# Kernel optimization log

Hardware: AMD Instinct MI355X
Metric: run time of the kernel (lower is better)

## Reference

```python
import jax, jax.numpy as jnp
import numpy as np

N_NODES = 100000
N_EDGES = 800000


def gcn_layer(x, W, b, src, dst, n):
    # PyG GCNConv (normalize=True): x @ W, add self-loops, sym-normalized mean aggregation, + bias
    h = x @ W  # [N, out]
    deg = jax.ops.segment_sum(jnp.ones_like(src, dtype=h.dtype), dst, num_segments=n)
    dinv = jnp.where(deg > 0, jax.lax.rsqrt(jnp.maximum(deg, 1.0)), 0.0)
    norm = dinv[src] * dinv[dst]  # [E+N]
    msg = h[src] * norm[:, None]  # gather + scale
    out = jax.ops.segment_sum(msg, dst, num_segments=n)  # scatter-add
    return out + b


def setup_inputs() -> dict:
    key = jax.random.key(0)
    k1, k2, k3, k4 = jax.random.split(key, 4)
    x = jax.random.normal(k1, (N_NODES, 128), dtype=jnp.float32)
    edge_index = jax.random.randint(k2, (2, N_EDGES), 0, N_NODES, dtype=jnp.int64)
    W1 = jax.random.normal(k3, (128, 64), dtype=jnp.float32) * (1.0 / np.sqrt(128))
    b1 = jnp.zeros((64,), dtype=jnp.float32)
    W2 = jax.random.normal(k4, (64, 40), dtype=jnp.float32) * (1.0 / np.sqrt(64))
    b2 = jnp.zeros((40,), dtype=jnp.float32)
    return {"x": x, "edge_index": edge_index, "W1": W1, "b1": b1, "W2": W2, "b2": b2}


def reference(x, edge_index, W1, b1, W2, b2):
    n = x.shape[0]
    loop = jnp.arange(n, dtype=edge_index.dtype)
    src = jnp.concatenate([edge_index[0], loop])  # add self-loops
    dst = jnp.concatenate([edge_index[1], loop])
    h = jax.nn.relu(gcn_layer(x, W1, b1, src, dst, n))
    # dropout is identity in eval mode (self.training=False)
    out = gcn_layer(h, W2, b2, src, dst, n)
    return jax.nn.log_softmax(out, axis=1)
```

## Files before the change

kernel.cpp:

```cpp
#include <hip/hip_runtime.h>
#include <hip/hip_fp16.h>
#include <math.h>


typedef _Float16 f16x8 __attribute__((ext_vector_type(8)));
typedef float    f32x4 __attribute__((ext_vector_type(4)));

__global__ void zero_kernel(int* __restrict__ p, int n) {
    int i = blockIdx.x * blockDim.x + threadIdx.x;
    if (i < n) p[i] = 0;
}

static __device__ __forceinline__ void gemm1_tile(const float* __restrict__ X,
                                                  const float* __restrict__ W,
                                                  _Float16* __restrict__ H, int n,
                                                  int tile, _Float16* Ws ) {
    int t = threadIdx.x;
    int rowbase = tile * 64;

    for (int i = t; i < 2048; i += 256) {
        int k = i >> 4;
        int nn0 = (i & 15) * 4;
        float4 v = *reinterpret_cast<const float4*>(W + (size_t)k * 64 + nn0);
        const float* vp = reinterpret_cast<const float*>(&v);
#pragma unroll
        for (int j = 0; j < 4; ++j) {
            int nn = nn0 + j;
            Ws[nn * 128 + (k ^ ((nn & 7) << 3))] = (_Float16)vp[j];
        }
    }

    int w = t >> 6;
    int l = t & 63;
    int lr = l & 15;
    int lk = l >> 4;
    int arow = rowbase + 16 * w + lr;
    int ar = arow < n ? arow : n - 1;

    f16x8 a[4];
#pragma unroll
    for (int kc = 0; kc < 4; ++kc) {
        const float* xp = X + (size_t)ar * 128 + kc * 32 + lk * 8;
        float4 v0 = *reinterpret_cast<const float4*>(xp);
        float4 v1 = *reinterpret_cast<const float4*>(xp + 4);
        f16x8 hv = { (_Float16)v0.x, (_Float16)v0.y, (_Float16)v0.z, (_Float16)v0.w,
                     (_Float16)v1.x, (_Float16)v1.y, (_Float16)v1.z, (_Float16)v1.w };
        a[kc] = hv;
    }
    __syncthreads();

    f32x4 acc[4] = {};
#pragma unroll
    for (int nt = 0; nt < 4; ++nt) {
        int nrow = 16 * nt + lr;
#pragma unroll
        for (int kc = 0; kc < 4; ++kc) {
            int k8 = kc * 32 + lk * 8;
            f16x8 b = *reinterpret_cast<f16x8*>(&Ws[nrow * 128 + (k8 ^ ((nrow & 7) << 3))]);
            acc[nt] = __builtin_amdgcn_mfma_f32_16x16x32_f16(a[kc], b, acc[nt], 0, 0, 0);
        }
    }
#pragma unroll
    for (int nt = 0; nt < 4; ++nt) {
#pragma unroll
        for (int r = 0; r < 4; ++r) {
            int grow = rowbase + 16 * w + lk * 4 + r;
            if (grow < n) H[(size_t)grow * 64 + nt * 16 + lr] = (_Float16)acc[nt][r];
        }
    }
}

__global__ __launch_bounds__(256) void degrank_gemm1_kernel(
        const int* __restrict__ dst, int* __restrict__ degi, int* __restrict__ rank, int E,
        const float* __restrict__ X, const float* __restrict__ W,
        _Float16* __restrict__ H, int n, int nDeg) {
    __shared__ _Float16 Ws[64 * 128];
    int b = blockIdx.x;
    if (b < nDeg) {
        int base = b * 1024 + threadIdx.x;
        int d[4]; bool v[4];
#pragma unroll
        for (int u = 0; u < 4; ++u) {
            int e = base + u * 256;
            v[u] = e < E;
            d[u] = v[u] ? dst[e] : 0;
        }
        int r[4];
#pragma unroll
        for (int u = 0; u < 4; ++u)
            if (v[u]) r[u] = atomicAdd(&degi[d[u]], 1);
#pragma unroll
        for (int u = 0; u < 4; ++u)
            if (v[u]) rank[base + u * 256] = r[u];
    } else {
        gemm1_tile(X, W, H, n, b - nDeg, Ws);
    }
}

__global__ __launch_bounds__(256) void fill_gemm1_kernel(
        const int* __restrict__ src, const int* __restrict__ dst,
        const int* __restrict__ rank, const float* __restrict__ dinv,
        const int* __restrict__ rowstart, int2* __restrict__ csr, int E,
        const float* __restrict__ X, const float* __restrict__ W,
        _Float16* __restrict__ H, int n, int nFill, int tileOff) {
    __shared__ _Float16 Ws[64 * 128];
    int b = blockIdx.x;
    if (b < nFill) {
        int e = b * 256 + threadIdx.x;
        if (e >= E) return;
        int s = src[e], t = dst[e];
        float nrm = dinv[s] * dinv[t];
        unsigned short us = __half_as_ushort(__float2half_rn(nrm));
        int packed = (int)(((unsigned)us << 16) | us);
        int pos = rowstart[t] + rank[e];
        csr[pos] = make_int2(s, packed);
    } else {
        gemm1_tile(X, W, H, n, b - nFill + tileOff, Ws);
    }
}

__global__ __launch_bounds__(256) void blocksum_kernel(const int* __restrict__ degi,
                                                       int* __restrict__ partial, int n) {
    __shared__ int sm[256];
    int t = threadIdx.x;
    int base = blockIdx.x * 1024 + t * 4;
    int s = 0;
#pragma unroll
    for (int j = 0; j < 4; ++j) { int i = base + j; if (i < n) s += degi[i]; }
    sm[t] = s;
    __syncthreads();
    for (int off = 128; off > 0; off >>= 1) {
        if (t < off) sm[t] += sm[t + off];
        __syncthreads();
    }
    if (t == 0) partial[blockIdx.x] = sm[0];
}

__global__ __launch_bounds__(256) void offsets_kernel(int* __restrict__ degi,
                                                      const int* __restrict__ partial,
                                                      int* __restrict__ rowstart,
                                                      int n, int nb) {
    __shared__ int sm[256];
    __shared__ int pbase_s;
    int t = threadIdx.x;
    int pv = (t < nb) ? partial[t] : 0;
    sm[t] = pv;
    __syncthreads();
    for (int off = 1; off < 256; off <<= 1) {
        int x = (t >= off) ? sm[t - off] : 0;
        __syncthreads();
        sm[t] += x;
        __syncthreads();
    }
    if (t == 0) pbase_s = (blockIdx.x > 0) ? sm[blockIdx.x - 1] : 0;
    __syncthreads();
    int pbase = pbase_s;
    __syncthreads();

    int base = blockIdx.x * 1024 + t * 4;
    int v[4]; int s = 0;
#pragma unroll
    for (int j = 0; j < 4; ++j) { v[j] = (base + j < n) ? degi[base + j] : 0; s += v[j]; }
    sm[t] = s;
    __syncthreads();
    for (int off = 1; off < 256; off <<= 1) {
        int x = (t >= off) ? sm[t - off] : 0;
        __syncthreads();
        sm[t] += x;
        __syncthreads();
    }
    int run = pbase + (sm[t] - s);
#pragma unroll
    for (int j = 0; j < 4; ++j) {
        if (base + j < n) {
            rowstart[base + j] = run; run += v[j];
            ((float*)degi)[base + j] = rsqrtf((float)v[j] + 1.0f);
        }
    }
}

static __device__ __forceinline__ __half2 relu_h2(__half2 v) {
    unsigned u = *reinterpret_cast<unsigned*>(&v);
    unsigned neg = (u >> 15) & 0x00010001u;
    u &= ~(neg * 0xFFFFu);
    return *reinterpret_cast<__half2*>(&u);
}

template <bool RELU, bool BIAS>
__global__ __launch_bounds__(256) void gather64h_kernel(const __half* __restrict__ Hh,
                                                        const int2* __restrict__ csr,
                                                        const int* __restrict__ rowstart,
                                                        const float* __restrict__ dinv,
                                                        const float* __restrict__ b,
                                                        __half* __restrict__ Oh, int n, int E) {
    int gt = blockIdx.x * blockDim.x + threadIdx.x;
    int node = gt >> 3;
    if (node >= n) return;
    int fl = gt & 7;
    const float4* H4 = reinterpret_cast<const float4*>(Hh);
    int rs = rowstart[node];
    int re = (node + 1 < n) ? rowstart[node + 1] : E;
    __half2 acc[4];
#pragma unroll
    for (int q = 0; q < 4; ++q) acc[q] = __float2half2_rn(0.0f);

    int e = rs;
    while (__any(e < re)) {
        int srcrow[4]; __half2 nh[4]; float4 raw[4];
#pragma unroll
        for (int u = 0; u < 4; ++u) {
            int ee = e + u;
            bool valid = ee < re;
            int2 c = csr[valid ? ee : rs];
            srcrow[u] = valid ? c.x : 0;
            int ni = valid ? c.y : 0;
            nh[u] = *reinterpret_cast<__half2*>(&ni);
        }
#pragma unroll
        for (int u = 0; u < 4; ++u)
            raw[u] = H4[srcrow[u] * 8 + fl];
#pragma unroll
        for (int u = 0; u < 4; ++u) {
            const __half2* hp = reinterpret_cast<const __half2*>(&raw[u]);
#pragma unroll
            for (int q = 0; q < 4; ++q)
                acc[q] = __hfma2(hp[q], nh[u], acc[q]);
        }
        e += 4;
    }
    {
        float di = dinv[node];
        __half2 d2 = __float2half2_rn(di * di);
        float4 raw = H4[node * 8 + fl];
        const __half2* hp = reinterpret_cast<const __half2*>(&raw);
#pragma unroll
        for (int q = 0; q < 4; ++q) acc[q] = __hfma2(hp[q], d2, acc[q]);
    }
    if (BIAS) {
        float4 b0 = reinterpret_cast<const float4*>(b)[fl * 2];
        float4 b1 = reinterpret_cast<const float4*>(b)[fl * 2 + 1];
        acc[0] = __hadd2(acc[0], __float22half2_rn(make_float2(b0.x, b0.y)));
        acc[1] = __hadd2(acc[1], __float22half2_rn(make_float2(b0.z, b0.w)));
        acc[2] = __hadd2(acc[2], __float22half2_rn(make_float2(b1.x, b1.y)));
        acc[3] = __hadd2(acc[3], __float22half2_rn(make_float2(b1.z, b1.w)));
    }
    if (RELU) {
#pragma unroll
        for (int q = 0; q < 4; ++q) acc[q] = relu_h2(acc[q]);
    }
    float4 o;
    __half2* op = reinterpret_cast<__half2*>(&o);
#pragma unroll
    for (int q = 0; q < 4; ++q) op[q] = acc[q];
    *reinterpret_cast<float4*>(Oh + (size_t)node * 64 + fl * 8) = o;
}

__global__ __launch_bounds__(256) void gather_gemm2_softmax(
        const __half* __restrict__ Hh, const int2* __restrict__ csr,
        const int* __restrict__ rowstart, const float* __restrict__ dinv,
        const float* __restrict__ W, const float* __restrict__ b,
        float* __restrict__ out, int n, int E) {
    constexpr int BM = 64, K = 64, C = 40, XP = 68, HP = 41;
    __shared__ float Xs[BM * XP];
    __shared__ float Ws[K * C];
    __shared__ float bs[C];
    __shared__ float rowm[BM], rowls[BM];
    int t = threadIdx.x;
    int rowbase = blockIdx.x * BM;

    for (int i = t; i < K * C / 4; i += 256)
        ((float4*)Ws)[i] = ((const float4*)W)[i];
    if (t < C) bs[t] = b[t];

    int team = t >> 3, fl = t & 7;
    const float4* H4 = reinterpret_cast<const float4*>(Hh);
#pragma unroll
    for (int pass = 0; pass < 2; ++pass) {
        int lrow = team + pass * 32;
        int node = rowbase + lrow;
        __half2 acc[4];
#pragma unroll
        for (int q = 0; q < 4; ++q) acc[q] = __float2half2_rn(0.0f);
        if (node < n) {
            int rs = rowstart[node];
            int re = (node + 1 < n) ? rowstart[node + 1] : E;
            int e = rs;
            while (__any(e < re)) {
                int srcrow[4]; __half2 nh[4]; float4 raw[4];
#pragma unroll
                for (int u = 0; u < 4; ++u) {
                    int ee = e + u;
                    bool valid = ee < re;
                    int2 c = csr[valid ? ee : rs];
                    srcrow[u] = valid ? c.x : 0;
                    int ni = valid ? c.y : 0;
                    nh[u] = *reinterpret_cast<__half2*>(&ni);
                }
#pragma unroll
                for (int u = 0; u < 4; ++u)
                    raw[u] = H4[srcrow[u] * 8 + fl];
#pragma unroll
                for (int u = 0; u < 4; ++u) {
                    const __half2* hp = reinterpret_cast<const __half2*>(&raw[u]);
#pragma unroll
                    for (int q = 0; q < 4; ++q)
                        acc[q] = __hfma2(hp[q], nh[u], acc[q]);
                }
                e += 4;
            }
            float di = dinv[node];
            __half2 d2 = __float2half2_rn(di * di);
            float4 raw = H4[node * 8 + fl];
            const __half2* hp = reinterpret_cast<const __half2*>(&raw);
#pragma unroll
            for (int q = 0; q < 4; ++q) acc[q] = __hfma2(hp[q], d2, acc[q]);
        }
        float* dp = &Xs[lrow * XP + fl * 8];
        float2 f0 = __half22float2(acc[0]), f1 = __half22float2(acc[1]);
        float2 f2 = __half22float2(acc[2]), f3 = __half22float2(acc[3]);
        *reinterpret_cast<float4*>(dp)     = make_float4(f0.x, f0.y, f1.x, f1.y);
        *reinterpret_cast<float4*>(dp + 4) = make_float4(f2.x, f2.y, f3.x, f3.y);
    }
    __syncthreads();

    int tx = t % (C / 4);
    int ty = t / (C / 4);
    bool active = ty < BM / 4;
    float acc[4][4] = {};
    if (active) {
#pragma unroll
        for (int k0 = 0; k0 < K; k0 += 4) {
            float4 xq[4], wq[4];
#pragma unroll
            for (int i = 0; i < 4; ++i)
                xq[i] = *reinterpret_cast<const float4*>(&Xs[(ty * 4 + i) * XP + k0]);
#pragma unroll
            for (int j = 0; j < 4; ++j)
                wq[j] = *reinterpret_cast<const float4*>(&Ws[(k0 + j) * C + tx * 4]);
#pragma unroll
            for (int i = 0; i < 4; ++i) {
                const float* xa = reinterpret_cast<const float*>(&xq[i]);
#pragma unroll
                for (int j = 0; j < 4; ++j) {
                    const float* wb = reinterpret_cast<const float*>(&wq[j]);
                    acc[i][0] += xa[j] * wb[0];
                    acc[i][1] += xa[j] * wb[1];
                    acc[i][2] += xa[j] * wb[2];
                    acc[i][3] += xa[j] * wb[3];
                }
            }
        }
    }
    __syncthreads();
    float* Hs = Xs;
    if (active) {
#pragma unroll
        for (int i = 0; i < 4; ++i) {
            int r = ty * 4 + i;
#pragma unroll
            for (int j = 0; j < 4; ++j)
                Hs[r * HP + tx * 4 + j] = acc[i][j] + bs[tx * 4 + j];
        }
    }
    __syncthreads();
    if (t < BM) {
        float m = -INFINITY;
        for (int j = 0; j < C; ++j) m = fmaxf(m, Hs[t * HP + j]);
        float s = 0.f;
        for (int j = 0; j < C; ++j) s += __expf(Hs[t * HP + j] - m);
        rowm[t] = m; rowls[t] = __logf(s);
    }
    __syncthreads();
    for (int idx = t; idx < BM * C; idx += 256) {
        int r = idx / C, c = idx - r * C;
        int gr = rowbase + r;
        if (gr < n) out[(size_t)gr * C + c] = Hs[r * HP + c] - rowm[r] - rowls[r];
    }
}

extern "C" void kernel_launch(void* const* d_in, const int* in_sizes, int n_in,
                              void* d_out, int out_size, void* d_ws, size_t ws_size,
                              hipStream_t stream) {
    const float* x  = (const float*)d_in[0];
    const int*   ei = (const int*)d_in[1];
    const float* W1 = (const float*)d_in[2];
    const float* b1 = (const float*)d_in[3];
    const float* W2 = (const float*)d_in[4];
    const float* b2 = (const float*)d_in[5];
    float* out = (float*)d_out;

    const int n = in_sizes[0] / 128;
    const int E = in_sizes[1] / 2;
    const int* src = ei;
    const int* dst = ei + E;

    auto al = [](size_t x) { return (x + 255) & ~(size_t)255; };
    float* ws = (float*)d_ws;
    size_t o_deg  = 0;
    size_t o_cnt  = al(n);
    size_t o_part = o_cnt + al(n);
    size_t o_rank = o_part + 1024;
    size_t o_csr  = o_rank + al(E);
    size_t o_h1   = o_csr + al((size_t)2 * E);
    size_t o_out1 = o_h1 + al((size_t)n * 32);

    int*    degi     = (int*)(ws + o_deg);
    float*  dinv     = (float*)(ws + o_deg);
    int*    rowstart = (int*)(ws + o_cnt);
    int*    partial  = (int*)(ws + o_part);
    int*    rank     = (int*)(ws + o_rank);
    int2*   csr      = (int2*)(ws + o_csr);
    __half* h1       = (__half*)(ws + o_h1);
    __half* out1     = (__half*)(ws + o_out1);

    const int NB = (n + 1023) / 1024;
    const int nDeg   = (E + 1023) / 1024;
    const int nFill  = (E + 255) / 256;
    const int ntiles = (n + 63) / 64;
    const int tilesA = ntiles / 2;
    const int tilesB = ntiles - tilesA;

    zero_kernel<<<(n + 255) / 256, 256, 0, stream>>>(degi, n);
    degrank_gemm1_kernel<<<nDeg + tilesA, 256, 0, stream>>>(
        dst, degi, rank, E, x, W1, (_Float16*)h1, n, nDeg);
    blocksum_kernel<<<NB, 256, 0, stream>>>(degi, partial, n);
    offsets_kernel<<<NB, 256, 0, stream>>>(degi, partial, rowstart, n, NB);
    fill_gemm1_kernel<<<nFill + tilesB, 256, 0, stream>>>(
        src, dst, rank, dinv, rowstart, csr, E, x, W1, (_Float16*)h1, n, nFill, tilesA);
    gather64h_kernel<true, true><<<((size_t)n * 8 + 255) / 256, 256, 0, stream>>>(
        h1, csr, rowstart, dinv, b1, out1, n, E);
    gather_gemm2_softmax<<<(n + 63) / 64, 256, 0, stream>>>(
        out1, csr, rowstart, dinv, W2, b2, out, n, E);
}
```

Baseline: 136.7 us.

## Privatize degree histogram per XCD with workgroup-scope atomics

Replaces the single global degree histogram with eight per-XCD copies, chosen via the hardware XCC id register. Atomics use workgroup scope so they can stay in the local XCD L2 instead of going device-coherent. A later pass combines the per-XCD counts into totals and per-XCD base offsets, and the CSR fill adds the XCD base to each edge's local rank, which is stored with the XCD id in its top bits. This adds 8x histogram zeroing and a reduction pass, plus extra memory traffic, in exchange for cheaper atomics.

```diff
diff --git a/kernel.cpp b/kernel.cpp
--- a/kernel.cpp
+++ b/kernel.cpp
@@ -5,6 +5,10 @@
 
 typedef _Float16 f16x8 __attribute__((ext_vector_type(8)));
 typedef float    f32x4 __attribute__((ext_vector_type(4)));
+
+static __device__ __forceinline__ int xcd_id() {
+    return __builtin_amdgcn_s_getreg((3 << 11) | 20) & 7;
+}
 
 __global__ void zero_kernel(int* __restrict__ p, int n) {
     int i = blockIdx.x * blockDim.x + threadIdx.x;
@@ -71,12 +75,14 @@
 }
 
 __global__ __launch_bounds__(256) void degrank_gemm1_kernel(
-        const int* __restrict__ dst, int* __restrict__ degi, int* __restrict__ rank, int E,
-        const float* __restrict__ X, const float* __restrict__ W,
-        _Float16* __restrict__ H, int n, int nDeg) {
+        const int* __restrict__ dst, int* __restrict__ degi_x, int* __restrict__ rank,
+        int E, int n, const float* __restrict__ X, const float* __restrict__ W,
+        _Float16* __restrict__ H, int nDeg) {
     __shared__ _Float16 Ws[64 * 128];
     int b = blockIdx.x;
     if (b < nDeg) {
+        int x = xcd_id();
+        int* hist = degi_x + (size_t)x * n;
         int base = b * 1024 + threadIdx.x;
         int d[4]; bool v[4];
 #pragma unroll
@@ -88,21 +94,98 @@
         int r[4];
 #pragma unroll
         for (int u = 0; u < 4; ++u)
-            if (v[u]) r[u] = atomicAdd(&degi[d[u]], 1);
+            if (v[u]) r[u] = __hip_atomic_fetch_add(&hist[d[u]], 1, __ATOMIC_RELAXED,
+                                                    __HIP_MEMORY_SCOPE_WORKGROUP);
 #pragma unroll
         for (int u = 0; u < 4; ++u)
-            if (v[u]) rank[base + u * 256] = r[u];
+            if (v[u]) rank[base + u * 256] = (x << 28) | r[u];
     } else {
         gemm1_tile(X, W, H, n, b - nDeg, Ws);
+    }
+}
+
+__global__ __launch_bounds__(256) void blocksum_kernel(const int* __restrict__ degi_x,
+                                                       int* __restrict__ base_x,
+                                                       int* __restrict__ degtot,
+                                                       int* __restrict__ partial, int n) {
+    __shared__ int sm[256];
+    int t = threadIdx.x;
+    int base = blockIdx.x * 1024 + t * 4;
+    int s = 0;
+#pragma unroll
+    for (int j = 0; j < 4; ++j) {
+        int i = base + j;
+        if (i < n) {
+            int running = 0;
+#pragma unroll
+            for (int x = 0; x < 8; ++x) {
+                int v = degi_x[(size_t)x * n + i];
+                base_x[(size_t)x * n + i] = running;
+                running += v;
+            }
+            degtot[i] = running;
+            s += running;
+        }
+    }
+    sm[t] = s;
+    __syncthreads();
+    for (int off = 128; off > 0; off >>= 1) {
+        if (t < off) sm[t] += sm[t + off];
+        __syncthreads();
+    }
+    if (t == 0) partial[blockIdx.x] = sm[0];
+}
+
+__global__ __launch_bounds__(256) void offsets_kernel(int* __restrict__ degtot,
+                                                      const int* __restrict__ partial,
+                                                      int* __restrict__ rowstart,
+                                                      int n, int nb) {
+    __shared__ int sm[256];
+    __shared__ int pbase_s;
+    int t = threadIdx.x;
+    int pv = (t < nb) ? partial[t] : 0;
+    sm[t] = pv;
+    __syncthreads();
+    for (int off = 1; off < 256; off <<= 1) {
+        int x = (t >= off) ? sm[t - off] : 0;
+        __syncthreads();
+        sm[t] += x;
+        __syncthreads();
+    }
+    if (t == 0) pbase_s = (blockIdx.x > 0) ? sm[blockIdx.x - 1] : 0;
+    __syncthreads();
+    int pbase = pbase_s;
+    __syncthreads();
+
+    int base = blockIdx.x * 1024 + t * 4;
+    int v[4]; int s = 0;
+#pragma unroll
+    for (int j = 0; j < 4; ++j) { v[j] = (base + j < n) ? degtot[base + j] : 0; s += v[j]; }
+    sm[t] = s;
+    __syncthreads();
+    for (int off = 1; off < 256; off <<= 1) {
+        int x = (t >= off) ? sm[t - off] : 0;
+        __syncthreads();
+        sm[t] += x;
+        __syncthreads();
+    }
+    int run = pbase + (sm[t] - s);
+#pragma unroll
+    for (int j = 0; j < 4; ++j) {
+        if (base + j < n) {
+            rowstart[base + j] = run; run += v[j];
+            ((float*)degtot)[base + j] = rsqrtf((float)v[j] + 1.0f);
+        }
     }
 }
 
 __global__ __launch_bounds__(256) void fill_gemm1_kernel(
         const int* __restrict__ src, const int* __restrict__ dst,
         const int* __restrict__ rank, const float* __restrict__ dinv,
-        const int* __restrict__ rowstart, int2* __restrict__ csr, int E,
+        const int* __restrict__ rowstart, const int* __restrict__ base_x,
+        int2* __restrict__ csr, int E, int n,
         const float* __restrict__ X, const float* __restrict__ W,
-        _Float16* __restrict__ H, int n, int nFill, int tileOff) {
+        _Float16* __restrict__ H, int nFill, int tileOff) {
     __shared__ _Float16 Ws[64 * 128];
     int b = blockIdx.x;
     if (b < nFill) {
@@ -112,70 +195,13 @@
         float nrm = dinv[s] * dinv[t];
         unsigned short us = __half_as_ushort(__float2half_rn(nrm));
         int packed = (int)(((unsigned)us << 16) | us);
-        int pos = rowstart[t] + rank[e];
+        int rk = rank[e];
+        int x = (unsigned)rk >> 28;
+        int lr = rk & 0x0FFFFFFF;
+        int pos = rowstart[t] + base_x[(size_t)x * n + t] + lr;
         csr[pos] = make_int2(s, packed);
     } else {
         gemm1_tile(X, W, H, n, b - nFill + tileOff, Ws);
-    }
-}
-
-__global__ __launch_bounds__(256) void blocksum_kernel(const int* __restrict__ degi,
-                                                       int* __restrict__ partial, int n) {
-    __shared__ int sm[256];
-    int t = threadIdx.x;
-    int base = blockIdx.x * 1024 + t * 4;
-    int s = 0;
-#pragma unroll
-    for (int j = 0; j < 4; ++j) { int i = base + j; if (i < n) s += degi[i]; }
-    sm[t] = s;
-    __syncthreads();
-    for (int off = 128; off > 0; off >>= 1) {
-        if (t < off) sm[t] += sm[t + off];
-        __syncthreads();
-    }
-    if (t == 0) partial[blockIdx.x] = sm[0];
-}
-
-__global__ __launch_bounds__(256) void offsets_kernel(int* __restrict__ degi,
-                                                      const int* __restrict__ partial,
-                                                      int* __restrict__ rowstart,
-                                                      int n, int nb) {
-    __shared__ int sm[256];
-    __shared__ int pbase_s;
-    int t = threadIdx.x;
-    int pv = (t < nb) ? partial[t] : 0;
-    sm[t] = pv;
-    __syncthreads();
-    for (int off = 1; off < 256; off <<= 1) {
-        int x = (t >= off) ? sm[t - off] : 0;
-        __syncthreads();
-        sm[t] += x;
-        __syncthreads();
-    }
-    if (t == 0) pbase_s = (blockIdx.x > 0) ? sm[blockIdx.x - 1] : 0;
-    __syncthreads();
-    int pbase = pbase_s;
-    __syncthreads();
-
-    int base = blockIdx.x * 1024 + t * 4;
-    int v[4]; int s = 0;
-#pragma unroll
-    for (int j = 0; j < 4; ++j) { v[j] = (base + j < n) ? degi[base + j] : 0; s += v[j]; }
-    sm[t] = s;
-    __syncthreads();
-    for (int off = 1; off < 256; off <<= 1) {
-        int x = (t >= off) ? sm[t - off] : 0;
-        __syncthreads();
-        sm[t] += x;
-        __syncthreads();
-    }
-    int run = pbase + (sm[t] - s);
-#pragma unroll
-    for (int j = 0; j < 4; ++j) {
-        if (base + j < n) {
-            rowstart[base + j] = run; run += v[j];
-            ((float*)degi)[base + j] = rsqrtf((float)v[j] + 1.0f);
-        }
     }
 }
 
@@ -394,18 +420,22 @@
     const int* src = ei;
     const int* dst = ei + E;
 
-    auto al = [](size_t x) { return (x + 255) & ~(size_t)255; };
+    auto al = [](size_t v) { return (v + 255) & ~(size_t)255; };
     float* ws = (float*)d_ws;
-    size_t o_deg  = 0;
-    size_t o_cnt  = al(n);
+    size_t o_degx = 0;
+    size_t o_basx = al((size_t)8 * n);
+    size_t o_degt = o_basx + al((size_t)8 * n);
+    size_t o_cnt  = o_degt + al(n);
     size_t o_part = o_cnt + al(n);
     size_t o_rank = o_part + 1024;
     size_t o_csr  = o_rank + al(E);
     size_t o_h1   = o_csr + al((size_t)2 * E);
     size_t o_out1 = o_h1 + al((size_t)n * 32);
 
-    int*    degi     = (int*)(ws + o_deg);
-    float*  dinv     = (float*)(ws + o_deg);
+    int*    degi_x   = (int*)(ws + o_degx);
+    int*    base_x   = (int*)(ws + o_basx);
+    int*    degtot   = (int*)(ws + o_degt);
+    float*  dinv     = (float*)(ws + o_degt);
     int*    rowstart = (int*)(ws + o_cnt);
     int*    partial  = (int*)(ws + o_part);
     int*    rank     = (int*)(ws + o_rank);
@@ -420,13 +450,14 @@
     const int tilesA = ntiles / 2;
     const int tilesB = ntiles - tilesA;
 
-    zero_kernel<<<(n + 255) / 256, 256, 0, stream>>>(degi, n);
+    zero_kernel<<<(8 * n + 255) / 256, 256, 0, stream>>>(degi_x, 8 * n);
     degrank_gemm1_kernel<<<nDeg + tilesA, 256, 0, stream>>>(
-        dst, degi, rank, E, x, W1, (_Float16*)h1, n, nDeg);
-    blocksum_kernel<<<NB, 256, 0, stream>>>(degi, partial, n);
-    offsets_kernel<<<NB, 256, 0, stream>>>(degi, partial, rowstart, n, NB);
+        dst, degi_x, rank, E, n, x, W1, (_Float16*)h1, nDeg);
+    blocksum_kernel<<<NB, 256, 0, stream>>>(degi_x, base_x, degtot, partial, n);
+    offsets_kernel<<<NB, 256, 0, stream>>>(degtot, partial, rowstart, n, NB);
     fill_gemm1_kernel<<<nFill + tilesB, 256, 0, stream>>>(
-        src, dst, rank, dinv, rowstart, csr, E, x, W1, (_Float16*)h1, n, nFill, tilesA);
+        src, dst, rank, dinv, rowstart, base_x, csr, E, n,
+        x, W1, (_Float16*)h1, nFill, tilesA);
     gather64h_kernel<true, true><<<((size_t)n * 8 + 255) / 256, 256, 0, stream>>>(
         h1, csr, rowstart, dinv, b1, out1, n, E);
     gather_gemm2_softmax<<<(n + 63) / 64, 256, 0, stream>>>(
```

Result: slower. 142.0 us (+3.9%).
